# Optimization experiments

Hardware: AMD Instinct MI355X
Metric: run time of the kernel (lower is better)

The kernel has to match this reference:

```python
import jax, jax.numpy as jnp
import numpy as np

THETA = 10000.0

def _rope(x, pos):
    # x: [b, h, s, hd]; pos: [s]
    hd = x.shape[-1]
    inv_freq = 1.0 / (THETA ** (jnp.arange(0, hd, 2, dtype=jnp.float32) / hd))  # [hd/2]
    ang = pos.astype(jnp.float32)[:, None] * inv_freq[None, :]                   # [s, hd/2]
    cos, sin = jnp.cos(ang), jnp.sin(ang)
    x1, x2 = x[..., 0::2], x[..., 1::2]
    r1 = x1 * cos - x2 * sin
    r2 = x1 * sin + x2 * cos
    return jnp.stack([r1, r2], axis=-1).reshape(x.shape)

def setup_inputs() -> dict:
    key = jax.random.key(0)
    ks = jax.random.split(key, 5)
    b, s, d = 2, 2048, 1024
    scale = 0.02
    return {
        "x": jax.random.normal(ks[0], (b, s, d), dtype=jnp.float32),
        "Wq": jax.random.normal(ks[1], (d, d), dtype=jnp.float32) * scale,
        "Wk": jax.random.normal(ks[2], (d, d), dtype=jnp.float32) * scale,
        "Wv": jax.random.normal(ks[3], (d, d), dtype=jnp.float32) * scale,
        "Wo": jax.random.normal(ks[4], (d, d), dtype=jnp.float32) * scale,
    }

def reference(x, Wq, Wk, Wv, Wo):
    b, s, d = x.shape
    n_heads = 16
    hd = d // n_heads

    def split_heads(t):  # [b,s,d] -> [b,h,s,hd]
        return t.reshape(b, s, n_heads, hd).transpose(0, 2, 1, 3)

    q = split_heads(x @ Wq.T)
    k = split_heads(x @ Wk.T)
    v = split_heads(x @ Wv.T)

    pos = jnp.arange(s)
    q = _rope(q, pos)
    k = _rope(k, pos)

    scores = jnp.einsum("bhqd,bhkd->bhqk", q, k) / jnp.sqrt(jnp.float32(hd))
    causal = jnp.tril(jnp.ones((s, s), dtype=bool))
    scores = jnp.where(causal, scores, -jnp.inf)
    attn = jax.nn.softmax(scores, axis=-1)
    ctx = jnp.einsum("bhqk,bhkd->bhqd", attn, v)
    ctx = ctx.transpose(0, 2, 1, 3).reshape(b, s, d)
    return ctx @ Wo.T
```

## Files before the change

### kernel.cpp

```cpp
#include <hip/hip_runtime.h>
#include <math.h>

#define B  2
#define S  2048
#define D  1024
#define NH 16
#define HD 64
#define NROWS (B * S)

#define AS1 __attribute__((address_space(1)))
#define AS3 __attribute__((address_space(3)))
#define GLD16(g, l) __builtin_amdgcn_global_load_lds((const AS1 void*)(g), (AS3 void*)(l), 16, 0, 0)

typedef __attribute__((ext_vector_type(8))) short short8;
typedef __attribute__((ext_vector_type(4))) float floatx4;

#define MFMA16(a, b, c) __builtin_amdgcn_mfma_f32_16x16x32_bf16((a), (b), (c), 0, 0, 0)

__device__ inline unsigned short f2bf(float f) {
    union { float f; unsigned int u; } v; v.f = f;
    unsigned int u = v.u;
    u += 0x7fffu + ((u >> 16) & 1);
    return (unsigned short)(u >> 16);
}

__global__ __launch_bounds__(256) void cvt_kernel(
    const float* __restrict__ x,  const float* __restrict__ Wq,
    const float* __restrict__ Wk, const float* __restrict__ Wv,
    const float* __restrict__ Wo,
    unsigned short* __restrict__ xb,  unsigned short* __restrict__ wqb,
    unsigned short* __restrict__ wkb, unsigned short* __restrict__ wvb,
    unsigned short* __restrict__ wob)
{
    size_t idx = (size_t)blockIdx.x * 256 + threadIdx.x;
    const float* src; unsigned short* dst; size_t off;
    if (idx < (1u << 20)) { src = x; dst = xb; off = idx << 2; }
    else {
        size_t r = idx - (1u << 20);
        int w = (int)(r >> 18);
        off = (r & ((1u << 18) - 1)) << 2;
        src = (w == 0) ? Wq : (w == 1) ? Wk : (w == 2) ? Wv : Wo;
        dst = (w == 0) ? wqb : (w == 1) ? wkb : (w == 2) ? wvb : wob;
    }
    float4 f = *(const float4*)(src + off);
    ushort4 o;
    o.x = f2bf(f.x); o.y = f2bf(f.y); o.z = f2bf(f.z); o.w = f2bf(f.w);
    *(ushort4*)(dst + off) = o;
}

__global__ __launch_bounds__(256) void gemm_qkv_mfma(
    const unsigned short* __restrict__ xb,
    const unsigned short* __restrict__ wqb,
    const unsigned short* __restrict__ wkb,
    const unsigned short* __restrict__ wvb,
    unsigned short* __restrict__ Qo, unsigned short* __restrict__ Ko,
    unsigned short* __restrict__ Vo)
{
    __shared__ short As[128 * 32];
    __shared__ short Bs[128 * 32];

    const int t    = threadIdx.x;
    const int wave = t >> 6, lane = t & 63;
    const int i0   = blockIdx.x * 128;
    const int by   = blockIdx.y;
    const int mat  = by >> 3;
    const int j0   = (by & 7) * 128;
    const unsigned short* __restrict__ W = (mat == 0) ? wqb : (mat == 1) ? wkb : wvb;
    unsigned short* __restrict__ out = (mat == 0) ? Qo : (mat == 1) ? Ko : Vo;

    const int wm = (wave & 1) * 64, wn = (wave >> 1) * 64;
    const int lm = lane & 15, quad = lane >> 4;

    const int seg0 = wave * 2;
    const int c0   = seg0 * 64 + lane;
    const int row0 = c0 >> 2, ko0 = (c0 & 3) << 3;
    const int c1   = c0 + 64;
    const int row1 = c1 >> 2, ko1 = (c1 & 3) << 3;

    const unsigned short* Abase = xb + (size_t)i0 * D;
    const unsigned short* Bbase = W  + (size_t)j0 * D;

    floatx4 acc[4][4] = {};

    for (int k0 = 0; k0 < D; k0 += 32) {
        __syncthreads();
        GLD16(Abase + (size_t)row0 * D + k0 + ko0, As + seg0 * 512);
        GLD16(Abase + (size_t)row1 * D + k0 + ko1, As + (seg0 + 1) * 512);
        GLD16(Bbase + (size_t)row0 * D + k0 + ko0, Bs + seg0 * 512);
        GLD16(Bbase + (size_t)row1 * D + k0 + ko1, Bs + (seg0 + 1) * 512);
        __syncthreads();

        short8 a[4], b[4];
        #pragma unroll
        for (int mi = 0; mi < 4; ++mi)
            a[mi] = *(const short8*)&As[(wm + mi * 16 + lm) * 32 + quad * 8];
        #pragma unroll
        for (int ni = 0; ni < 4; ++ni)
            b[ni] = *(const short8*)&Bs[(wn + ni * 16 + lm) * 32 + quad * 8];
        #pragma unroll
        for (int mi = 0; mi < 4; ++mi)
            #pragma unroll
            for (int ni = 0; ni < 4; ++ni)
                acc[mi][ni] = MFMA16(a[mi], b[ni], acc[mi][ni]);
    }

    #pragma unroll
    for (int ni = 0; ni < 4; ++ni) {
        const int nw  = j0 + wn + ni * 16 + lm;
        const int h   = nw >> 6, dim = nw & 63;
        float invf = 0.0f;
        if (mat < 2)
            invf = exp2f(-(float)(dim & ~1) * (13.287712379549449f / 64.0f));
        #pragma unroll
        for (int mi = 0; mi < 4; ++mi) {
            #pragma unroll
            for (int r = 0; r < 4; ++r) {
                const int mg = i0 + wm + mi * 16 + quad * 4 + r;
                const int si = mg & (S - 1), bb = mg >> 11;
                float v = acc[mi][ni][r];
                float res;
                if (mat < 2) {
                    float pv = __shfl_xor(v, 1);
                    float sn, cs;
                    __sincosf((float)si * invf, &sn, &cs);
                    res = (lane & 1) ? (pv * sn + v * cs) : (v * cs - pv * sn);
                    if (mat == 0) res *= 0.1803368801111204f;
                } else {
                    res = v;
                }
                out[((size_t)(bb * NH + h) * S + si) * HD + dim] = f2bf(res);
            }
        }
    }
}

__global__ __launch_bounds__(256) void gemm_out_mfma(
    const unsigned short* __restrict__ Cb,
    const unsigned short* __restrict__ wob,
    float* __restrict__ out)
{
    __shared__ short As[128 * 32];
    __shared__ short Bs[128 * 32];

    const int t    = threadIdx.x;
    const int wave = t >> 6, lane = t & 63;
    const int i0   = blockIdx.x * 128;
    const int j0   = blockIdx.y * 128;

    const int wm = (wave & 1) * 64, wn = (wave >> 1) * 64;
    const int lm = lane & 15, quad = lane >> 4;

    const int seg0 = wave * 2;
    const int c0   = seg0 * 64 + lane;
    const int row0 = c0 >> 2, ko0 = (c0 & 3) << 3;
    const int c1   = c0 + 64;
    const int row1 = c1 >> 2, ko1 = (c1 & 3) << 3;

    const unsigned short* Abase = Cb  + (size_t)i0 * D;
    const unsigned short* Bbase = wob + (size_t)j0 * D;

    floatx4 acc[4][4] = {};

    for (int k0 = 0; k0 < D; k0 += 32) {
        __syncthreads();
        GLD16(Abase + (size_t)row0 * D + k0 + ko0, As + seg0 * 512);
        GLD16(Abase + (size_t)row1 * D + k0 + ko1, As + (seg0 + 1) * 512);
        GLD16(Bbase + (size_t)row0 * D + k0 + ko0, Bs + seg0 * 512);
        GLD16(Bbase + (size_t)row1 * D + k0 + ko1, Bs + (seg0 + 1) * 512);
        __syncthreads();

        short8 a[4], b[4];
        #pragma unroll
        for (int mi = 0; mi < 4; ++mi)
            a[mi] = *(const short8*)&As[(wm + mi * 16 + lm) * 32 + quad * 8];
        #pragma unroll
        for (int ni = 0; ni < 4; ++ni)
            b[ni] = *(const short8*)&Bs[(wn + ni * 16 + lm) * 32 + quad * 8];
        #pragma unroll
        for (int mi = 0; mi < 4; ++mi)
            #pragma unroll
            for (int ni = 0; ni < 4; ++ni)
                acc[mi][ni] = MFMA16(a[mi], b[ni], acc[mi][ni]);
    }

    #pragma unroll
    for (int ni = 0; ni < 4; ++ni) {
        const int ng = j0 + wn + ni * 16 + lm;
        #pragma unroll
        for (int mi = 0; mi < 4; ++mi) {
            #pragma unroll
            for (int r = 0; r < 4; ++r) {
                const int mg = i0 + wm + mi * 16 + quad * 4 + r;
                out[(size_t)mg * D + ng] = acc[mi][ni][r];
            }
        }
    }
}

__global__ __launch_bounds__(256) void vtrans_kernel(
    const unsigned short* __restrict__ Vb, unsigned short* __restrict__ Vt)
{
    __shared__ unsigned short T[64][72];
    const int t  = threadIdx.x;
    const int st = blockIdx.x, bh = blockIdx.y;
    const unsigned short* src = Vb + ((size_t)bh * S + st * 64) * HD;

    #pragma unroll
    for (int i = 0; i < 2; ++i) {
        int c = t + i * 256;
        int s = c & 63, dp = c >> 6;
        short8 v = *(const short8*)(src + (size_t)s * HD + dp * 8);
        #pragma unroll
        for (int j = 0; j < 8; ++j)
            T[dp * 8 + j][s] = (unsigned short)v[j];
    }
    __syncthreads();
    unsigned short* dst = Vt + (size_t)bh * HD * S + (size_t)st * 64;
    #pragma unroll
    for (int i = 0; i < 2; ++i) {
        int c = t + i * 256;
        int d = c >> 3, sp = (c & 7) * 8;
        short8 v = *(const short8*)&T[d][sp];
        *(short8*)(dst + (size_t)d * S + sp) = v;
    }
}

#define ATTN_STEP(KC, VC, KN, VN)                                              \
{                                                                              \
    _Pragma("unroll")                                                          \
    for (int i = 0; i < 2; ++i) {                                              \
        int c = t + i * 256;                                                   \
        int row = c >> 3;                                                      \
        int dkc = (c & 7) ^ (row & 7);                                         \
        GLD16(Kg + (size_t)(k0n + row) * HD + dkc * 8, &KN[0][0] + c * 8);     \
        GLD16(Vg + (size_t)row * S + k0n + dkc * 8,    &VN[0][0] + c * 8);     \
    }                                                                          \
    short8 kb0[4], kb1[4];                                                     \
    _Pragma("unroll")                                                          \
    for (int nt = 0; nt < 4; ++nt) {                                           \
        kb0[nt] = *(const short8*)&KC[nt * 16 + lm][(quad ^ sw) * 8];          \
        kb1[nt] = *(const short8*)&KC[nt * 16 + lm][((4 + quad) ^ sw) * 8];    \
    }                                                                          \
    floatx4 sc[4];                                                             \
    _Pragma("unroll")                                                          \
    for (int nt = 0; nt < 4; ++nt) {                                           \
        floatx4 s = {0.f, 0.f, 0.f, 0.f};                                      \
        s = MFMA16(qa0, kb0[nt], s);                                           \
        s = MFMA16(qa1, kb1[nt], s);                                           \
        sc[nt] = s;                                                            \
    }                                                                          \
    if (diag) {                                                                \
        _Pragma("unroll")                                                      \
        for (int r = 0; r < 4; ++r)                                            \
            _Pragma("unroll")                                                  \
            for (int nt = 0; nt < 4; ++nt) {                                   \
                float pe = exp2f(sc[nt][r]);                                   \
                if (nt * 16 + lm > 16 * wave + quad * 4 + r) pe = 0.0f;        \
                sc[nt][r] = pe;                                                \
                lsum[r] += pe;                                                 \
            }                                                                  \
    } else {                                                                   \
        _Pragma("unroll")                                                      \
        for (int r = 0; r < 4; ++r)                                            \
            _Pragma("unroll")                                                  \
            for (int nt = 0; nt < 4; ++nt) {                                   \
                float pe = exp2f(sc[nt][r]);                                   \
                sc[nt][r] = pe;                                                \
                lsum[r] += pe;                                                 \
            }                                                                  \
    }                                                                          \
    _Pragma("unroll")                                                          \
    for (int nt = 0; nt < 4; ++nt)                                             \
        _Pragma("unroll")                                                      \
        for (int r = 0; r < 4; ++r) {                                          \
            int q = 16 * wave + quad * 4 + r;                                  \
            Ps[q][(((nt * 2 + (lm >> 3)) ^ (q & 7)) * 8) + (lm & 7)] =         \
                f2bf(sc[nt][r]);                                               \
        }                                                                      \
    short8 pa0 = *(const short8*)&Ps[16 * wave + lm][(quad ^ sw) * 8];         \
    short8 pa1 = *(const short8*)&Ps[16 * wave + lm][((4 + quad) ^ sw) * 8];   \
    _Pragma("unroll")                                                          \
    for (int nt = 0; nt < 4; ++nt) {                                           \
        short8 vb0 = *(const short8*)&VC[nt * 16 + lm][(quad ^ sw) * 8];       \
        short8 vb1 = *(const short8*)&VC[nt * 16 + lm][((4 + quad) ^ sw) * 8]; \
        o[nt] = MFMA16(pa0, vb0, o[nt]);                                       \
        o[nt] = MFMA16(pa1, vb1, o[nt]);                                       \
    }                                                                          \
    __syncthreads();                                                           \
}

__global__ __launch_bounds__(256, 4) void attn_mfma(
    const unsigned short* __restrict__ Qb,
    const unsigned short* __restrict__ Kb,
    const unsigned short* __restrict__ Vt,
    unsigned short* __restrict__ Cb)
{
    __shared__ unsigned short Ks0[64][64];
    __shared__ unsigned short Ks1[64][64];
    __shared__ unsigned short Vs0[64][64];
    __shared__ unsigned short Vs1[64][64];
    __shared__ unsigned short Ps[64][64];

    const int t    = threadIdx.x;
    const int lane = t & 63, wave = t >> 6;
    const int lm   = lane & 15, quad = lane >> 4;
    const int sw   = lm & 7;

    const int b     = blockIdx.x;
    const int bh    = b & 31;
    const int f     = (b >> 5) & 7;
    const int round = b >> 8;
    int qt;
    if      (round == 0) qt = f;
    else if (round == 1) qt = 15 - f;
    else if (round == 2) qt = 16 + f;
    else                 qt = 31 - f;
    const int q0 = qt * 64;

    const unsigned short* Qg = Qb + (size_t)bh * S * HD;
    const unsigned short* Kg = Kb + (size_t)bh * S * HD;
    const unsigned short* Vg = Vt + (size_t)bh * HD * S;

    short8 qa0 = *(const short8*)(Qg + (size_t)(q0 + 16 * wave + lm) * HD + quad * 8);
    short8 qa1 = *(const short8*)(Qg + (size_t)(q0 + 16 * wave + lm) * HD + 32 + quad * 8);

    #pragma unroll
    for (int i = 0; i < 2; ++i) {
        int c = t + i * 256;
        int row = c >> 3;
        int dkc = (c & 7) ^ (row & 7);
        GLD16(Kg + (size_t)row * HD + dkc * 8, &Ks0[0][0] + c * 8);
        GLD16(Vg + (size_t)row * S + dkc * 8,  &Vs0[0][0] + c * 8);
    }

    float lsum[4] = {0.f, 0.f, 0.f, 0.f};
    floatx4 o[4] = {};

    __syncthreads();

    for (int kt = 0; kt <= qt; ++kt) {
        const int k0n = (kt + 1) * 64;
        const bool diag = (kt == qt);
        if ((kt & 1) == 0) ATTN_STEP(Ks0, Vs0, Ks1, Vs1)
        else               ATTN_STEP(Ks1, Vs1, Ks0, Vs0)
    }

    #pragma unroll
    for (int r = 0; r < 4; ++r) {
        #pragma unroll
        for (int off = 1; off < 16; off <<= 1)
            lsum[r] += __shfl_xor(lsum[r], off);
    }
    const int h = bh & (NH - 1), bb = bh >> 4;
    #pragma unroll
    for (int r = 0; r < 4; ++r) {
        float inv = 1.0f / lsum[r];
        size_t row = (size_t)bb * S + q0 + 16 * wave + quad * 4 + r;
        #pragma unroll
        for (int nt = 0; nt < 4; ++nt)
            Cb[row * D + h * HD + nt * 16 + lm] = f2bf(o[nt][r] * inv);
    }
}

extern "C" void kernel_launch(void* const* d_in, const int* in_sizes, int n_in,
                              void* d_out, int out_size, void* d_ws, size_t ws_size,
                              hipStream_t stream) {
    (void)in_sizes; (void)n_in; (void)out_size; (void)ws_size;
    const float* x  = (const float*)d_in[0];
    const float* Wq = (const float*)d_in[1];
    const float* Wk = (const float*)d_in[2];
    const float* Wv = (const float*)d_in[3];
    const float* Wo = (const float*)d_in[4];
    float* out = (float*)d_out;

    char* w = (char*)d_ws;
    unsigned short* Qb  = (unsigned short*)(w);
    unsigned short* Kb  = (unsigned short*)(w + (((size_t)8)  << 20));
    unsigned short* Vb  = (unsigned short*)(w + (((size_t)16) << 20));
    unsigned short* Vtb = (unsigned short*)(w + (((size_t)24) << 20));
    unsigned short* Cb  = (unsigned short*)(w + (((size_t)32) << 20));
    unsigned short* xb  = (unsigned short*)(w + (((size_t)40) << 20));
    unsigned short* wqb = (unsigned short*)(w + (((size_t)48) << 20));
    unsigned short* wkb = (unsigned short*)(w + (((size_t)50) << 20));
    unsigned short* wvb = (unsigned short*)(w + (((size_t)52) << 20));
    unsigned short* wob = (unsigned short*)(w + (((size_t)54) << 20));

    cvt_kernel<<<8192, 256, 0, stream>>>(x, Wq, Wk, Wv, Wo,
                                         xb, wqb, wkb, wvb, wob);

    dim3 g1(NROWS / 128, 24);
    gemm_qkv_mfma<<<g1, 256, 0, stream>>>(xb, wqb, wkb, wvb, Qb, Kb, Vb);

    dim3 gt(S / 64, B * NH);
    vtrans_kernel<<<gt, 256, 0, stream>>>(Vb, Vtb);

    attn_mfma<<<1024, 256, 0, stream>>>(Qb, Kb, Vtb, Cb);

    dim3 g3(NROWS / 128, D / 128);
    gemm_out_mfma<<<g3, 256, 0, stream>>>(Cb, wob, out);
}
```

Measured before the change: 207.4 us.

## Double-buffer LDS in projection GEMMs and vectorize epilogue stores via swapped MFMA operands

Both the QKV and output projection GEMMs now ping-pong between two LDS buffers, so the async global-to-LDS load of the next K slice is issued before the MFMAs on the current slice. This halves the barriers per K step and overlaps memory with compute. MFMA operands are swapped so each lane holds four consecutive output columns. RoPE pairs then sit in-register without a shuffle, and stores become packed ushort4/float4 writes instead of scalar strided ones. The cost is twice the LDS per block, which could lower occupancy.

After: 192.8 us. -7.1%, faster.

```diff
diff --git a/kernel.cpp b/kernel.cpp
--- a/kernel.cpp
+++ b/kernel.cpp
@@ -48,6 +48,30 @@
     *(ushort4*)(dst + off) = o;
 }
 
+#define GEMM_STAGE(Abase, Bbase, kk, AD, BD)                                   \
+{                                                                              \
+    GLD16(Abase + (size_t)row0 * D + (kk) + ko0, AD + seg0 * 512);             \
+    GLD16(Abase + (size_t)row1 * D + (kk) + ko1, AD + (seg0 + 1) * 512);       \
+    GLD16(Bbase + (size_t)row0 * D + (kk) + ko0, BD + seg0 * 512);             \
+    GLD16(Bbase + (size_t)row1 * D + (kk) + ko1, BD + (seg0 + 1) * 512);       \
+}
+
+#define GEMM_COMPUTE(AC, BC)                                                   \
+{                                                                              \
+    short8 a[4], b[4];                                                         \
+    _Pragma("unroll")                                                          \
+    for (int mi = 0; mi < 4; ++mi)                                             \
+        a[mi] = *(const short8*)&AC[(wm + mi * 16 + lm) * 32 + quad * 8];      \
+    _Pragma("unroll")                                                          \
+    for (int ni = 0; ni < 4; ++ni)                                             \
+        b[ni] = *(const short8*)&BC[(wn + ni * 16 + lm) * 32 + quad * 8];      \
+    _Pragma("unroll")                                                          \
+    for (int mi = 0; mi < 4; ++mi)                                             \
+        _Pragma("unroll")                                                      \
+        for (int ni = 0; ni < 4; ++ni)                                         \
+            acc[mi][ni] = MFMA16(b[ni], a[mi], acc[mi][ni]);      \
+}
+
 __global__ __launch_bounds__(256) void gemm_qkv_mfma(
     const unsigned short* __restrict__ xb,
     const unsigned short* __restrict__ wqb,
@@ -56,8 +80,10 @@
     unsigned short* __restrict__ Qo, unsigned short* __restrict__ Ko,
     unsigned short* __restrict__ Vo)
 {
-    __shared__ short As[128 * 32];
-    __shared__ short Bs[128 * 32];
+    __shared__ short As0[128 * 32];
+    __shared__ short As1[128 * 32];
+    __shared__ short Bs0[128 * 32];
+    __shared__ short Bs1[128 * 32];
 
     const int t    = threadIdx.x;
     const int wave = t >> 6, lane = t & 63;
@@ -82,54 +108,52 @@
 
     floatx4 acc[4][4] = {};
 
-    for (int k0 = 0; k0 < D; k0 += 32) {
+    GEMM_STAGE(Abase, Bbase, 0, As0, Bs0);
+    __syncthreads();
+    for (int k0 = 0; k0 < D; k0 += 64) {
+        GEMM_STAGE(Abase, Bbase, k0 + 32, As1, Bs1);
+        GEMM_COMPUTE(As0, Bs0);
         __syncthreads();
-        GLD16(Abase + (size_t)row0 * D + k0 + ko0, As + seg0 * 512);
-        GLD16(Abase + (size_t)row1 * D + k0 + ko1, As + (seg0 + 1) * 512);
-        GLD16(Bbase + (size_t)row0 * D + k0 + ko0, Bs + seg0 * 512);
-        GLD16(Bbase + (size_t)row1 * D + k0 + ko1, Bs + (seg0 + 1) * 512);
+        if (k0 + 64 < D) GEMM_STAGE(Abase, Bbase, k0 + 64, As0, Bs0);
+        GEMM_COMPUTE(As1, Bs1);
         __syncthreads();
-
-        short8 a[4], b[4];
+    }
+
+    const int h = (j0 + wn) >> 6;
+    #pragma unroll
+    for (int mi = 0; mi < 4; ++mi) {
+        const int mg = i0 + wm + mi * 16 + lm;
+        const int si = mg & (S - 1), bb = mg >> 11;
+        unsigned short* orow = out + ((size_t)(bb * NH + h) * S + si) * HD;
         #pragma unroll
-        for (int mi = 0; mi < 4; ++mi)
-            a[mi] = *(const short8*)&As[(wm + mi * 16 + lm) * 32 + quad * 8];
-        #pragma unroll
-        for (int ni = 0; ni < 4; ++ni)
-            b[ni] = *(const short8*)&Bs[(wn + ni * 16 + lm) * 32 + quad * 8];
-        #pragma unroll
-        for (int mi = 0; mi < 4; ++mi)
-            #pragma unroll
-            for (int ni = 0; ni < 4; ++ni)
-                acc[mi][ni] = MFMA16(a[mi], b[ni], acc[mi][ni]);
-    }
-
-    #pragma unroll
-    for (int ni = 0; ni < 4; ++ni) {
-        const int nw  = j0 + wn + ni * 16 + lm;
-        const int h   = nw >> 6, dim = nw & 63;
-        float invf = 0.0f;
-        if (mat < 2)
-            invf = exp2f(-(float)(dim & ~1) * (13.287712379549449f / 64.0f));
-        #pragma unroll
-        for (int mi = 0; mi < 4; ++mi) {
-            #pragma unroll
-            for (int r = 0; r < 4; ++r) {
-                const int mg = i0 + wm + mi * 16 + quad * 4 + r;
-                const int si = mg & (S - 1), bb = mg >> 11;
-                float v = acc[mi][ni][r];
-                float res;
-                if (mat < 2) {
-                    float pv = __shfl_xor(v, 1);
+        for (int ni = 0; ni < 4; ++ni) {
+            const int dim0 = ni * 16 + quad * 4;
+            floatx4 v = acc[mi][ni];
+            ushort4 pk;
+            if (mat < 2) {
+                float rv[4];
+                #pragma unroll
+                for (int p = 0; p < 2; ++p) {
+                    float invf = exp2f(-(float)(dim0 + 2 * p) *
+                                       (13.287712379549449f / 64.0f));
                     float sn, cs;
                     __sincosf((float)si * invf, &sn, &cs);
-                    res = (lane & 1) ? (pv * sn + v * cs) : (v * cs - pv * sn);
-                    if (mat == 0) res *= 0.1803368801111204f;
-                } else {
-                    res = v;
+                    float x1 = v[2 * p], x2 = v[2 * p + 1];
+                    float r1 = x1 * cs - x2 * sn;
+                    float r2 = x1 * sn + x2 * cs;
+                    if (mat == 0) {
+                        r1 *= 0.1803368801111204f;
+                        r2 *= 0.1803368801111204f;
+                    }
+                    rv[2 * p] = r1; rv[2 * p + 1] = r2;
                 }
-                out[((size_t)(bb * NH + h) * S + si) * HD + dim] = f2bf(res);
+                pk.x = f2bf(rv[0]); pk.y = f2bf(rv[1]);
+                pk.z = f2bf(rv[2]); pk.w = f2bf(rv[3]);
+            } else {
+                pk.x = f2bf(v[0]); pk.y = f2bf(v[1]);
+                pk.z = f2bf(v[2]); pk.w = f2bf(v[3]);
             }
+            *(ushort4*)(orow + dim0) = pk;
         }
     }
 }
@@ -139,8 +163,10 @@
     const unsigned short* __restrict__ wob,
     float* __restrict__ out)
 {
-    __shared__ short As[128 * 32];
-    __shared__ short Bs[128 * 32];
+    __shared__ short As0[128 * 32];
+    __shared__ short As1[128 * 32];
+    __shared__ short Bs0[128 * 32];
+    __shared__ short Bs1[128 * 32];
 
     const int t    = threadIdx.x;
     const int wave = t >> 6, lane = t & 63;
@@ -161,38 +187,25 @@
 
     floatx4 acc[4][4] = {};
 
-    for (int k0 = 0; k0 < D; k0 += 32) {
+    GEMM_STAGE(Abase, Bbase, 0, As0, Bs0);
+    __syncthreads();
+    for (int k0 = 0; k0 < D; k0 += 64) {
+        GEMM_STAGE(Abase, Bbase, k0 + 32, As1, Bs1);
+        GEMM_COMPUTE(As0, Bs0);
         __syncthreads();
-        GLD16(Abase + (size_t)row0 * D + k0 + ko0, As + seg0 * 512);
-        GLD16(Abase + (size_t)row1 * D + k0 + ko1, As + (seg0 + 1) * 512);
-        GLD16(Bbase + (size_t)row0 * D + k0 + ko0, Bs + seg0 * 512);
-        GLD16(Bbase + (size_t)row1 * D + k0 + ko1, Bs + (seg0 + 1) * 512);
+        if (k0 + 64 < D) GEMM_STAGE(Abase, Bbase, k0 + 64, As0, Bs0);
+        GEMM_COMPUTE(As1, Bs1);
         __syncthreads();
-
-        short8 a[4], b[4];
+    }
+
+    #pragma unroll
+    for (int mi = 0; mi < 4; ++mi) {
+        const int mg = i0 + wm + mi * 16 + lm;
+        float* orow = out + (size_t)mg * D;
         #pragma unroll
-        for (int mi = 0; mi < 4; ++mi)
-            a[mi] = *(const short8*)&As[(wm + mi * 16 + lm) * 32 + quad * 8];
-        #pragma unroll
-        for (int ni = 0; ni < 4; ++ni)
-            b[ni] = *(const short8*)&Bs[(wn + ni * 16 + lm) * 32 + quad * 8];
-        #pragma unroll
-        for (int mi = 0; mi < 4; ++mi)
-            #pragma unroll
-            for (int ni = 0; ni < 4; ++ni)
-                acc[mi][ni] = MFMA16(a[mi], b[ni], acc[mi][ni]);
-    }
-
-    #pragma unroll
-    for (int ni = 0; ni < 4; ++ni) {
-        const int ng = j0 + wn + ni * 16 + lm;
-        #pragma unroll
-        for (int mi = 0; mi < 4; ++mi) {
-            #pragma unroll
-            for (int r = 0; r < 4; ++r) {
-                const int mg = i0 + wm + mi * 16 + quad * 4 + r;
-                out[(size_t)mg * D + ng] = acc[mi][ni][r];
-            }
+        for (int ni = 0; ni < 4; ++ni) {
+            const int ng = j0 + wn + ni * 16 + quad * 4;
+            *(floatx4*)(orow + ng) = acc[mi][ni];
         }
     }
 }
```
